# Kernel optimization log

Measured on AMD Instinct MI355X. Metric: run time of the kernel, lower is better.

## Reference

```python
import jax, jax.numpy as jnp
import numpy as np

D, K, STRIDE, PADDING = 5, 3, 1, 2
B, CIN, COUT, H, W = 32, 128, 256, 56, 56


def _conv(x, w, stride, padding):
    return jax.lax.conv_general_dilated(
        x, w, window_strides=(stride, stride),
        padding=[(padding, padding), (padding, padding)],
        dimension_numbers=("NCHW", "OIHW", "NCHW"))


def setup_inputs() -> dict:
    key = jax.random.key(0)
    k1, k2, k3 = jax.random.split(key, 3)
    x = jax.random.normal(k1, (B, CIN, H, W), dtype=jnp.float32)
    # kaiming-uniform-ish core init
    fan_in = CIN * K * K
    bound = float(np.sqrt(6.0 / fan_in))
    core = jax.random.uniform(k2, (COUT, CIN, K, K), dtype=jnp.float32,
                              minval=-bound, maxval=bound)
    periphery = jax.random.uniform(k3, (D * D - K * K,), dtype=jnp.float32,
                                   minval=-0.1, maxval=0.1)
    thresh = jnp.ones((COUT,), jnp.float32) * 0.1
    scale = jnp.array([10.0], jnp.float32)
    return {"x": x, "core": core, "periphery": periphery,
            "thresh": thresh, "scale": scale}


def reference(x, core, periphery, thresh, scale):
    pad = (D - K) // 2  # offset of the KxK core inside the DxD window
    # Dense core conv: embed KxK core at the center of a DxD kernel so core
    # and periphery share the same output grid (padding=PADDING for DxD).
    core_full = jnp.pad(core, ((0, 0), (0, 0), (pad, pad), (pad, pad)))
    core_out = _conv(x, core_full, STRIDE, PADDING)  # [B, COUT, Ho, Wo]

    # Periphery: one shared scalar per off-core offset, shared across all
    # in/out channels -> sum input over channels, conv with a 1x1-channel
    # DxD stencil whose core region is zero.
    periph_mask = np.ones((D, D), dtype=bool)
    periph_mask[pad:pad + K, pad:pad + K] = False
    periph_idx = np.flatnonzero(periph_mask)  # row-major off-core offsets
    pk = jnp.zeros((D * D,), x.dtype).at[periph_idx].set(periphery)
    pk = pk.reshape(1, 1, D, D)
    xs = jnp.sum(x, axis=1, keepdims=True)  # [B,1,H,W]
    periph_out = _conv(xs, pk, STRIDE, PADDING)  # [B,1,Ho,Wo]

    # Per-out-channel threshold/scale gating: periphery term is switched on
    # where the core response exceeds the channel threshold (soft gate).
    gate = jax.nn.sigmoid(scale[0] * (core_out - thresh[None, :, None, None]))
    return core_out + gate * periph_out
```

## Files before the change

kernel.cpp:

```cpp
#include <hip/hip_runtime.h>

typedef __attribute__((__ext_vector_type__(8))) _Float16 f16x8;
typedef __attribute__((__ext_vector_type__(4))) float f32x4;
typedef __attribute__((__ext_vector_type__(4))) int i32x4;

#define HW 56
#define HW2 3136
#define CIN 128
#define COUT 256
#define NB 32
#define NPIX 100352
#define PH 58

static __device__ __forceinline__ unsigned short f2h(float f) {
  _Float16 h = (_Float16)f;
  return __builtin_bit_cast(unsigned short, h);
}

#define GLD_LDS16(g, l)                                          \
  __builtin_amdgcn_global_load_lds(                              \
      (const __attribute__((address_space(1))) void*)(g),        \
      (__attribute__((address_space(3))) void*)(l), 16, 0, 0)

__global__ __launch_bounds__(256) void prep_x(const float* __restrict__ x,
                                              unsigned short* __restrict__ xp,
                                              float* __restrict__ xs) {
  if (blockIdx.x >= NB * HW) {
    int t = (blockIdx.x - NB * HW) * 256 + threadIdx.x;
    int ck = t & 15;
    int pi = t >> 4;
    int b = pi / 228, r = pi - b * 228;
    int h, w;
    if (r < 58) { h = 0; w = r; }
    else if (r < 116) { h = 57; w = r - 58; }
    else { int q = r - 116; h = 1 + (q >> 1); w = (q & 1) * 57; }
    size_t off = (((size_t)(b * PH + h) * PH + w) << 8) + (ck << 4);
    *reinterpret_cast<i32x4*>((char*)xp + off) = (i32x4){0, 0, 0, 0};
    return;
  }
  __shared__ float tile[CIN * 57];
  const int bh = blockIdx.x;
  const float* src = x + (size_t)(bh / HW) * CIN * HW2 + (size_t)(bh % HW) * HW;
  for (int idx = threadIdx.x; idx < CIN * HW; idx += 256) {
    int c = idx / HW, w = idx - c * HW;
    tile[c * 57 + w] = src[(size_t)c * HW2 + w];
  }
  __syncthreads();
  unsigned short* dst =
      xp + (((size_t)(bh / HW) * PH + (bh % HW) + 1) * PH + 1) * CIN;
  for (int idx = threadIdx.x; idx < HW * (CIN / 2); idx += 256) {
    int w = idx >> 6;
    int c = (idx & 63) << 1;
    unsigned lo = f2h(tile[c * 57 + w]);
    unsigned hi = f2h(tile[(c + 1) * 57 + w]);
    *reinterpret_cast<unsigned*>(&dst[w * CIN + c]) = lo | (hi << 16);
  }
  if (threadIdx.x < HW) {
    float s = 0.f;
    for (int c = 0; c < CIN; ++c) s += tile[c * 57 + threadIdx.x];
    xs[(size_t)bh * HW + threadIdx.x] = s;
  }
}

__global__ __launch_bounds__(256) void prep_w(const float* __restrict__ core,
                                              unsigned short* __restrict__ w_t) {
  int i = blockIdx.x * 256 + threadIdx.x;
  int c = i & 127;
  int p = (i >> 7) % 9;
  int m = i / (9 * 128);
  w_t[i] = f2h(core[(size_t)(m * CIN + c) * 9 + p]);
}

__global__ __launch_bounds__(256) void periph_k(const float* __restrict__ xs,
                                                const float* __restrict__ per,
                                                float* __restrict__ po) {
  int n = blockIdx.x * 256 + threadIdx.x;
  int b = n / HW2, r = n - b * HW2;
  int ho = r / HW, wo = r - ho * HW;
  const float* xb = xs + (size_t)b * HW2;
  const int pdy[16] = {0,0,0,0,0,1,1,2,2,3,3,4,4,4,4,4};
  const int pdx[16] = {0,1,2,3,4,0,4,0,4,0,4,0,1,2,3,4};
  float acc = 0.f;
#pragma unroll
  for (int t = 0; t < 16; ++t) {
    int h = ho + pdy[t] - 2, w = wo + pdx[t] - 2;
    if ((unsigned)h < HW && (unsigned)w < HW) acc += per[t] * xb[h * HW + w];
  }
  po[n] = acc;
}

__global__ __launch_bounds__(256, 2) void gemm_k(const unsigned short* __restrict__ xp,
                                                 const unsigned short* __restrict__ w_t,
                                                 const float* __restrict__ po,
                                                 const float* __restrict__ thresh,
                                                 const float* __restrict__ scale,
                                                 float* __restrict__ out) {
  __shared__ __align__(16) char sMem[2 * 32768];

  const int tid = threadIdx.x;
  const int lane = tid & 63;
  const int wid = tid >> 6;
  const int wm = wid >> 1;
  const int wn = wid & 1;

  const int bid = blockIdx.x;
  const int sb = (bid & 7) * 196 + (bid >> 3);
  const int m0 = (sb & 1) << 7;
  const int n0 = (sb >> 1) << 7;

  const int l8 = lane >> 3;
  const int ls = lane & 7;
  const int sw = (ls ^ l8) << 4;
  const char* xpc = (const char*)xp;
  const char* wtc = (const char*)w_t;
  const int aSrc0 = (m0 + wid * 32 + l8) * 2304 + sw;
  int bSrc[4];
#pragma unroll
  for (int c = 0; c < 4; ++c) {
    int n = n0 + wid * 32 + c * 8 + l8;
    int b = n / HW2, rr = n - b * HW2;
    int h = rr / HW, w = rr - h * HW;
    bSrc[c] = ((b * PH + h + 1) * PH + (w + 1)) * 256 + sw;
  }
  const int aDst = wid * 4096;
  const int bDst = 16384 + wid * 4096;

  int aro[4][2], bro[4][2];
#pragma unroll
  for (int i = 0; i < 4; ++i)
#pragma unroll
    for (int ko = 0; ko < 2; ++ko) {
      int rowA = wm * 64 + i * 16 + (lane & 15);
      int rowB = wn * 64 + i * 16 + (lane & 15);
      int boc = ko * 64 + ((lane >> 4) << 4);
      aro[i][ko] = rowA * 128 + (boc ^ ((rowA & 7) << 4));
      bro[i][ko] = 16384 + rowB * 128 + (boc ^ ((rowB & 7) << 4));
    }

  auto STAGE = [&](int buf, int t) {
    const int p = t >> 1;
    const int ch = (t & 1) << 7;
    const int dy = p / 3 - 1, dx = p - (p / 3) * 3 - 1;
    const int offA = (p << 8) + ch;
    const int offB = ((dy * PH + dx) << 8) + ch;
    char* base = sMem + buf * 32768;
#pragma unroll
    for (int c = 0; c < 4; ++c)
      GLD_LDS16(wtc + aSrc0 + c * 18432 + offA, base + aDst + c * 1024);
#pragma unroll
    for (int c = 0; c < 4; ++c)
      GLD_LDS16(xpc + bSrc[c] + offB, base + bDst + c * 1024);
  };

  f32x4 acc[4][4] = {};

  STAGE(0, 0);
  __syncthreads();

  for (int t = 0; t < 18; ++t) {
    const char* base = sMem + (t & 1) * 32768;
    __builtin_amdgcn_s_barrier();
    if (t < 17) {
      STAGE((t + 1) & 1, t + 1);
      asm volatile("s_waitcnt vmcnt(8)" ::: "memory");
    } else {
      asm volatile("s_waitcnt vmcnt(0)" ::: "memory");
    }
    __builtin_amdgcn_s_barrier();

    f16x8 bfr[4][2];
#pragma unroll
    for (int j = 0; j < 4; ++j)
#pragma unroll
      for (int ko = 0; ko < 2; ++ko)
        bfr[j][ko] = *reinterpret_cast<const f16x8*>(base + bro[j][ko]);
#pragma unroll
    for (int i = 0; i < 4; ++i) {
      f16x8 a0 = *reinterpret_cast<const f16x8*>(base + aro[i][0]);
      f16x8 a1 = *reinterpret_cast<const f16x8*>(base + aro[i][1]);
      __builtin_amdgcn_s_setprio(1);
#pragma unroll
      for (int j = 0; j < 4; ++j) {
        acc[i][j] = __builtin_amdgcn_mfma_f32_16x16x32_f16(a0, bfr[j][0], acc[i][j], 0, 0, 0);
        acc[i][j] = __builtin_amdgcn_mfma_f32_16x16x32_f16(a1, bfr[j][1], acc[i][j], 0, 0, 0);
      }
      __builtin_amdgcn_s_setprio(0);
    }
  }

  const float sc = scale[0];
#pragma unroll
  for (int j = 0; j < 4; ++j) {
    int n = n0 + wn * 64 + j * 16 + (lane & 15);
    int b = n / HW2;
    int r = n - b * HW2;
    float pv = po[n];
    float* op = out + (size_t)b * (COUT * HW2) + r;
#pragma unroll
    for (int i = 0; i < 4; ++i) {
      int cl = m0 + wm * 64 + i * 16 + ((lane >> 4) << 2);
      f32x4 th = *reinterpret_cast<const f32x4*>(&thresh[cl]);
#pragma unroll
      for (int q = 0; q < 4; ++q) {
        float cv = acc[i][j][q];
        float g = 1.f / (1.f + __expf(-sc * (cv - th[q])));
        op[(size_t)(cl + q) * HW2] = cv + g * pv;
      }
    }
  }
}

extern "C" void kernel_launch(void* const* d_in, const int* in_sizes, int n_in,
                              void* d_out, int out_size, void* d_ws, size_t ws_size,
                              hipStream_t stream) {
  (void)in_sizes; (void)n_in; (void)out_size; (void)ws_size;
  const float* x      = (const float*)d_in[0];
  const float* core   = (const float*)d_in[1];
  const float* per    = (const float*)d_in[2];
  const float* thresh = (const float*)d_in[3];
  const float* scale  = (const float*)d_in[4];
  float* out = (float*)d_out;

  char* ws = (char*)d_ws;
  unsigned short* xp  = (unsigned short*)ws;
  unsigned short* w_t = (unsigned short*)(ws + 27557888);
  float* xs           = (float*)(ws + 28147712);
  float* po           = (float*)(ws + 28549120);

  prep_x<<<NB * HW + 456, 256, 0, stream>>>(x, xp, xs);
  prep_w<<<(COUT * 9 * CIN) / 256, 256, 0, stream>>>(core, w_t);
  periph_k<<<NPIX / 256, 256, 0, stream>>>(xs, per, po);
  gemm_k<<<2 * (NPIX / 128), 256, 0, stream>>>(xp, w_t, po, thresh, scale, out);
}
```

Baseline: 113.0 us.

## Load weight fragments directly to registers from pre-swizzled layout, halve LDS

Weights are pre-packed into MFMA fragment order, so each lane fetches its A operand straight from global memory into registers with one 16-byte load per fragment. The weight tile no longer goes through shared memory, which halves LDS use and lets launch bounds request 3 blocks per CU. In exchange every wave issues its own redundant global loads of weights, relying on L1/L2 hits. The vmcnt waits are adjusted for the extra outstanding loads.

```diff
diff --git a/kernel.cpp b/kernel.cpp
--- a/kernel.cpp
+++ b/kernel.cpp
@@ -62,13 +62,23 @@
   }
 }
 
-__global__ __launch_bounds__(256) void prep_w(const float* __restrict__ core,
-                                              unsigned short* __restrict__ w_t) {
-  int i = blockIdx.x * 256 + threadIdx.x;
-  int c = i & 127;
-  int p = (i >> 7) % 9;
-  int m = i / (9 * 128);
-  w_t[i] = f2h(core[(size_t)(m * CIN + c) * 9 + p]);
+__global__ __launch_bounds__(256) void prep_w2(const float* __restrict__ core,
+                                               unsigned short* __restrict__ w_t2) {
+  int tid = blockIdx.x * 256 + threadIdx.x;
+  int l = tid & 63;
+  int c_id = tid >> 6;
+  int ko = c_id & 1;
+  int cb = (c_id >> 1) & 15;
+  int pc = c_id >> 5;
+  int ch = pc & 1, p = pc >> 1;
+  int cout = cb * 16 + (l & 15);
+  int chan0 = ch * 64 + ko * 32 + (l >> 4) * 8;
+  unsigned short v[8];
+#pragma unroll
+  for (int e = 0; e < 8; ++e)
+    v[e] = f2h(core[(size_t)(cout * CIN + chan0 + e) * 9 + p]);
+  *reinterpret_cast<i32x4*>(w_t2 + (size_t)tid * 8) =
+      *reinterpret_cast<const i32x4*>(v);
 }
 
 __global__ __launch_bounds__(256) void periph_k(const float* __restrict__ xs,
@@ -89,13 +99,13 @@
   po[n] = acc;
 }
 
-__global__ __launch_bounds__(256, 2) void gemm_k(const unsigned short* __restrict__ xp,
-                                                 const unsigned short* __restrict__ w_t,
+__global__ __launch_bounds__(256, 3) void gemm_k(const unsigned short* __restrict__ xp,
+                                                 const unsigned short* __restrict__ w_t2,
                                                  const float* __restrict__ po,
                                                  const float* __restrict__ thresh,
                                                  const float* __restrict__ scale,
                                                  float* __restrict__ out) {
-  __shared__ __align__(16) char sMem[2 * 32768];
+  __shared__ __align__(16) char sMem[2 * 16384];
 
   const int tid = threadIdx.x;
   const int lane = tid & 63;
@@ -112,8 +122,6 @@
   const int ls = lane & 7;
   const int sw = (ls ^ l8) << 4;
   const char* xpc = (const char*)xp;
-  const char* wtc = (const char*)w_t;
-  const int aSrc0 = (m0 + wid * 32 + l8) * 2304 + sw;
   int bSrc[4];
 #pragma unroll
   for (int c = 0; c < 4; ++c) {
@@ -122,49 +130,56 @@
     int h = rr / HW, w = rr - h * HW;
     bSrc[c] = ((b * PH + h + 1) * PH + (w + 1)) * 256 + sw;
   }
-  const int aDst = wid * 4096;
-  const int bDst = 16384 + wid * 4096;
-
-  int aro[4][2], bro[4][2];
-#pragma unroll
-  for (int i = 0; i < 4; ++i)
+  const int bDst = wid * 4096;
+
+  const int cbase = (m0 >> 4) + wm * 4;
+  const char* wa = (const char*)w_t2 + (lane << 4);
+
+  int bro[4][2];
+#pragma unroll
+  for (int j = 0; j < 4; ++j)
 #pragma unroll
     for (int ko = 0; ko < 2; ++ko) {
-      int rowA = wm * 64 + i * 16 + (lane & 15);
-      int rowB = wn * 64 + i * 16 + (lane & 15);
+      int rowB = wn * 64 + j * 16 + (lane & 15);
       int boc = ko * 64 + ((lane >> 4) << 4);
-      aro[i][ko] = rowA * 128 + (boc ^ ((rowA & 7) << 4));
-      bro[i][ko] = 16384 + rowB * 128 + (boc ^ ((rowB & 7) << 4));
-    }
-
-  auto STAGE = [&](int buf, int t) {
+      bro[j][ko] = rowB * 128 + (boc ^ ((rowB & 7) << 4));
+    }
+
+  auto STAGEB = [&](int buf, int t) {
     const int p = t >> 1;
     const int ch = (t & 1) << 7;
     const int dy = p / 3 - 1, dx = p - (p / 3) * 3 - 1;
-    const int offA = (p << 8) + ch;
     const int offB = ((dy * PH + dx) << 8) + ch;
-    char* base = sMem + buf * 32768;
-#pragma unroll
-    for (int c = 0; c < 4; ++c)
-      GLD_LDS16(wtc + aSrc0 + c * 18432 + offA, base + aDst + c * 1024);
+    char* base = sMem + buf * 16384;
 #pragma unroll
     for (int c = 0; c < 4; ++c)
       GLD_LDS16(xpc + bSrc[c] + offB, base + bDst + c * 1024);
   };
 
+#define LOADA(A, t)                                                         \
+  {                                                                         \
+    _Pragma("unroll") for (int i_ = 0; i_ < 4; ++i_)                        \
+        _Pragma("unroll") for (int ko_ = 0; ko_ < 2; ++ko_)                 \
+        A[i_ * 2 + ko_] = *reinterpret_cast<const f16x8*>(                  \
+            wa + (size_t)(((t)*16 + cbase + i_) * 2 + ko_) * 1024);         \
+  }
+
   f32x4 acc[4][4] = {};
-
-  STAGE(0, 0);
+  f16x8 pa[8];
+
+  STAGEB(0, 0);
   __syncthreads();
 
   for (int t = 0; t < 18; ++t) {
-    const char* base = sMem + (t & 1) * 32768;
+    const char* base = sMem + (t & 1) * 16384;
     __builtin_amdgcn_s_barrier();
     if (t < 17) {
-      STAGE((t + 1) & 1, t + 1);
+      STAGEB((t + 1) & 1, t + 1);
+      LOADA(pa, t)
+      asm volatile("s_waitcnt vmcnt(12)" ::: "memory");
+    } else {
+      LOADA(pa, t)
       asm volatile("s_waitcnt vmcnt(8)" ::: "memory");
-    } else {
-      asm volatile("s_waitcnt vmcnt(0)" ::: "memory");
     }
     __builtin_amdgcn_s_barrier();
 
@@ -176,17 +191,16 @@
         bfr[j][ko] = *reinterpret_cast<const f16x8*>(base + bro[j][ko]);
 #pragma unroll
     for (int i = 0; i < 4; ++i) {
-      f16x8 a0 = *reinterpret_cast<const f16x8*>(base + aro[i][0]);
-      f16x8 a1 = *reinterpret_cast<const f16x8*>(base + aro[i][1]);
       __builtin_amdgcn_s_setprio(1);
 #pragma unroll
       for (int j = 0; j < 4; ++j) {
-        acc[i][j] = __builtin_amdgcn_mfma_f32_16x16x32_f16(a0, bfr[j][0], acc[i][j], 0, 0, 0);
-        acc[i][j] = __builtin_amdgcn_mfma_f32_16x16x32_f16(a1, bfr[j][1], acc[i][j], 0, 0, 0);
+        acc[i][j] = __builtin_amdgcn_mfma_f32_16x16x32_f16(pa[i * 2], bfr[j][0], acc[i][j], 0, 0, 0);
+        acc[i][j] = __builtin_amdgcn_mfma_f32_16x16x32_f16(pa[i * 2 + 1], bfr[j][1], acc[i][j], 0, 0, 0);
       }
       __builtin_amdgcn_s_setprio(0);
     }
   }
+#undef LOADA
 
   const float sc = scale[0];
 #pragma unroll
@@ -222,13 +236,13 @@
   float* out = (float*)d_out;
 
   char* ws = (char*)d_ws;
-  unsigned short* xp  = (unsigned short*)ws;
-  unsigned short* w_t = (unsigned short*)(ws + 27557888);
-  float* xs           = (float*)(ws + 28147712);
-  float* po           = (float*)(ws + 28549120);
+  unsigned short* xp   = (unsigned short*)ws;
+  unsigned short* w_t2 = (unsigned short*)(ws + 27557888);
+  float* xs            = (float*)(ws + 28147712);
+  float* po            = (float*)(ws + 28549120);
 
   prep_x<<<NB * HW + 456, 256, 0, stream>>>(x, xp, xs);
-  prep_w<<<(COUT * 9 * CIN) / 256, 256, 0, stream>>>(core, w_t);
+  prep_w2<<<(576 * 64) / 256, 256, 0, stream>>>(core, w_t2);
   periph_k<<<NPIX / 256, 256, 0, stream>>>(xs, per, po);
-  gemm_k<<<2 * (NPIX / 128), 256, 0, stream>>>(xp, w_t, po, thresh, scale, out);
-}
+  gemm_k<<<2 * (NPIX / 128), 256, 0, stream>>>(xp, w_t2, po, thresh, scale, out);
+}
```

Result: no change. 111.4 us (-1.4%).
